# Kernel optimization log

Measured on AMD Instinct MI355X. Metric: run time of the kernel, lower is better.

The kernel has to match this reference:

```python
import jax, jax.numpy as jnp
import numpy as np

N_NODES = 100000
N_EDGES = 1600000
D = 128


def setup_inputs() -> dict:
    key = jax.random.key(0)
    ks = jax.random.split(key, 10)
    features = jax.random.normal(ks[0], (N_NODES, D), dtype=jnp.float32)
    edge_index = jax.random.randint(ks[1], (2, N_EDGES), 0, N_NODES, dtype=jnp.int64)
    edge_weight = jax.random.uniform(ks[2], (N_EDGES,), dtype=jnp.float32)
    scale = 1.0 / np.sqrt(D)
    W1 = jax.random.normal(ks[3], (D, D), dtype=jnp.float32) * scale
    b1 = jnp.zeros((D,), dtype=jnp.float32)
    a1 = jnp.full((D,), 0.25, dtype=jnp.float32)  # PReLU init
    W2 = jax.random.normal(ks[4], (D, D), dtype=jnp.float32) * scale
    b2 = jnp.zeros((D,), dtype=jnp.float32)
    a2 = jnp.full((D,), 0.25, dtype=jnp.float32)
    return {"features": features, "edge_index": edge_index, "edge_weight": edge_weight,
            "W1": W1, "b1": b1, "a1": a1, "W2": W2, "b2": b2, "a2": a2}


def _gcn_norm(edge_index, edge_weight, n_nodes):
    # PyG GCNConv default: add self-loops (weight 1), symmetric normalization.
    src, dst = edge_index[0], edge_index[1]
    loop = jnp.arange(n_nodes, dtype=src.dtype)
    src = jnp.concatenate([src, loop])
    dst = jnp.concatenate([dst, loop])
    w = jnp.concatenate([edge_weight, jnp.ones((n_nodes,), edge_weight.dtype)])
    deg = jax.ops.segment_sum(w, dst, num_segments=n_nodes)  # in-degree (target)
    dis = jnp.where(deg > 0, jax.lax.rsqrt(deg), 0.0)
    norm = dis[src] * w * dis[dst]  # [E + N]
    return src, dst, norm


def _gcn_layer(x, W, b, src, dst, norm, n_nodes):
    h = x @ W                                 # [N, D] dense GEMM first (PyG order)
    msg = h[src] * norm[:, None]              # gather + scale, [E+N, D]
    out = jax.ops.segment_sum(msg, dst, num_segments=n_nodes)
    return out + b


def _prelu(x, a):
    return jnp.where(x >= 0, x, a * x)


def reference(features, edge_index, edge_weight, W1, b1, a1, W2, b2, a2):
    n = features.shape[0]
    src, dst, norm = _gcn_norm(edge_index, edge_weight, n)
    # dropout is identity in eval mode
    x = _prelu(_gcn_layer(features, W1, b1, src, dst, norm, n), a1)
    x = _prelu(_gcn_layer(x, W2, b2, src, dst, norm, n), a2)
    return x
```

## Files before the change

kernel.cpp:

```cpp
#include <hip/hip_runtime.h>
#include <cstdint>

#define NN 100000
#define NE 1600000
#define DD 128
#define NB 250
#define BSZ 400

typedef unsigned int uint;
typedef unsigned short ushort;
typedef unsigned long long u64;

typedef __attribute__((ext_vector_type(8))) short short8;
typedef __attribute__((ext_vector_type(4))) float floatx4;

__device__ inline uint f2bf(float f) {
    uint u = __float_as_uint(f);
    return (u + 0x7fffu + ((u >> 16) & 1u)) >> 16;
}


__global__ __launch_bounds__(256) void zero_bc(uint* __restrict__ bc) {
    if (threadIdx.x < NB) bc[threadIdx.x] = 0u;
}

__global__ __launch_bounds__(256) void bucket_hist(const int* __restrict__ dst,
                                                   uint* __restrict__ bc) {
    __shared__ uint h[NB];
    int tid = threadIdx.x;
    if (tid < NB) h[tid] = 0u;
    __syncthreads();
    int e0 = blockIdx.x * 8192 + tid;
#pragma unroll
    for (int k = 0; k < 32; ++k) {
        int e = e0 + 256 * k;
        if (e < NE) atomicAdd(&h[(uint)dst[e] / BSZ], 1u);
    }
    __syncthreads();
    if (tid < NB && h[tid]) atomicAdd(&bc[tid], h[tid]);
}

__global__ __launch_bounds__(256) void bucket_prefix(const uint* __restrict__ bc,
                                                     uint* __restrict__ bbase,
                                                     uint* __restrict__ bcur) {
    int lane = threadIdx.x;
    if (lane < 64) {
        uint v[4], s = 0;
#pragma unroll
        for (int k = 0; k < 4; ++k) {
            int i = lane * 4 + k;
            v[k] = (i < NB) ? bc[i] : 0u;
            s += v[k];
        }
        uint inc = s;
#pragma unroll
        for (int d = 1; d < 64; d <<= 1) {
            uint t = __shfl_up(inc, (unsigned)d, 64);
            if (lane >= d) inc += t;
        }
        uint run = inc - s;
#pragma unroll
        for (int k = 0; k < 4; ++k) {
            int i = lane * 4 + k;
            if (i < NB) { bbase[i] = run; bcur[i] = run; run += v[k]; }
        }
        if (lane == 63) bbase[NB] = run;
    }
}

__global__ __launch_bounds__(256) void bucket_append(const int* __restrict__ src,
                                                     const int* __restrict__ dst,
                                                     const float* __restrict__ w,
                                                     uint* __restrict__ bcur,
                                                     int2* __restrict__ etmp) {
    __shared__ uint h[NB];
    __shared__ uint res[NB];
    int tid = threadIdx.x;
    if (tid < NB) h[tid] = 0u;
    __syncthreads();
    int e0 = blockIdx.x * 4096 + tid;
    uint rank[16], bkt[16];
#pragma unroll
    for (int k = 0; k < 16; ++k) {
        int e = e0 + 256 * k;
        if (e < NE) {
            uint b = (uint)dst[e] / BSZ;
            bkt[k] = b;
            rank[k] = atomicAdd(&h[b], 1u);
        } else bkt[k] = 0xffffffffu;
    }
    __syncthreads();
    if (tid < NB) res[tid] = h[tid] ? atomicAdd(&bcur[tid], h[tid]) : 0u;
    __syncthreads();
#pragma unroll
    for (int k = 0; k < 16; ++k) {
        if (bkt[k] != 0xffffffffu) {
            int e = e0 + 256 * k;
            uint dl = (uint)dst[e] - bkt[k] * BSZ;
            uint wq = (uint)(w[e] * 8388608.0f);
            if (wq > 8388607u) wq = 8388607u;
            etmp[res[bkt[k]] + rank[k]] = make_int2(src[e], (int)((dl << 23) | wq));
        }
    }
}

__global__ __launch_bounds__(256) void bucket_build(const int2* __restrict__ etmp,
                                                    const uint* __restrict__ bbase,
                                                    float* __restrict__ dis,
                                                    int* __restrict__ hist_g,
                                                    int* __restrict__ rowstart,
                                                    int2* __restrict__ edges) {
    __shared__ u64   wc[BSZ];
    __shared__ uint  cur[BSZ];
    __shared__ float disl[BSZ];
    int tid = threadIdx.x;
    int b = blockIdx.x;
    int n0 = b * BSZ;
    for (int i = tid; i < BSZ; i += 256) wc[i] = 0ull;
    __syncthreads();
    uint base = bbase[b], end = bbase[b + 1];
    for (uint i = base + tid; i < end; i += 256) {
        uint y = (uint)etmp[i].y;
        uint dl = y >> 23;
        atomicAdd(&wc[dl], ((u64)1 << 40) | (u64)(y & 0x7fffffu));
    }
    __syncthreads();
    if (tid < 64) {
        uint v[7], s = 0;
#pragma unroll
        for (int k = 0; k < 7; ++k) {
            int i = tid * 7 + k;
            v[k] = (i < BSZ) ? (uint)(wc[i] >> 40) : 0u;
            s += v[k];
        }
        uint inc = s;
#pragma unroll
        for (int d = 1; d < 64; d <<= 1) {
            uint t = __shfl_up(inc, (unsigned)d, 64);
            if (tid >= d) inc += t;
        }
        uint run = inc - s;
#pragma unroll
        for (int k = 0; k < 7; ++k) {
            int i = tid * 7 + k;
            if (i < BSZ) { cur[i] = run; run += v[k]; }
        }
    }
    __syncthreads();
    for (int i = tid; i < BSZ; i += 256) {
        u64 v = wc[i];
        float wsum = (float)(v & 0xffffffffffull) * (1.0f / 8388608.0f);
        float ds = rsqrtf(1.0f + wsum);
        disl[i] = ds;
        dis[n0 + i] = ds;
        hist_g[n0 + i] = (int)(v >> 40);
        rowstart[n0 + i] = (int)(base + cur[i]);
    }
    __syncthreads();
    for (uint i = base + tid; i < end; i += 256) {
        int2 e = etmp[i];
        uint y = (uint)e.y;
        uint dl = y >> 23;
        float wv = (float)(y & 0x7fffffu) * (1.0f / 8388608.0f);
        uint p = atomicAdd(&cur[dl], 1u);
        float nrm = wv * disl[dl];
        edges[base + p] = make_int2(e.x, __float_as_int(nrm));
    }
}

#define WTS 136
#define NTILES ((NN + 63) / 64)

template <bool AF32>
__global__ __launch_bounds__(256) void gemm_mfma(const void* __restrict__ Xv,
                                                 const float* __restrict__ W,
                                                 const float* __restrict__ dis,
                                                 ushort* __restrict__ HB) {
    __shared__ ushort Wt[DD * WTS];
    int tid = threadIdx.x;
#pragma unroll
    for (int it = 0; it < 16; ++it) {
        int flat = (tid + it * 256) * 4;
        int k = flat >> 7, n = flat & 127;
        float4 wv = *(const float4*)&W[flat];
        Wt[(n + 0) * WTS + k] = (ushort)f2bf(wv.x);
        Wt[(n + 1) * WTS + k] = (ushort)f2bf(wv.y);
        Wt[(n + 2) * WTS + k] = (ushort)f2bf(wv.z);
        Wt[(n + 3) * WTS + k] = (ushort)f2bf(wv.w);
    }
    __syncthreads();

    int wave = tid >> 6, lane = tid & 63;
    int q = lane >> 4, l16 = lane & 15;

    for (int tile = blockIdx.x; tile < NTILES; tile += gridDim.x) {
        int row0 = tile * 64 + wave * 16;

        int arow = row0 + l16;
        if (arow >= NN) arow = NN - 1;
        short8 afr[4];
        if (AF32) {
            const float* xr = (const float*)Xv + (size_t)arow * DD + q * 8;
#pragma unroll
            for (int ks = 0; ks < 4; ++ks) {
                float4 f0 = *(const float4*)(xr + ks * 32);
                float4 f1 = *(const float4*)(xr + ks * 32 + 4);
                uint4 u;
                u.x = f2bf(f0.x) | (f2bf(f0.y) << 16);
                u.y = f2bf(f0.z) | (f2bf(f0.w) << 16);
                u.z = f2bf(f1.x) | (f2bf(f1.y) << 16);
                u.w = f2bf(f1.z) | (f2bf(f1.w) << 16);
                afr[ks] = __builtin_bit_cast(short8, u);
            }
        } else {
            const ushort* xr = (const ushort*)Xv + (size_t)arow * DD + q * 8;
#pragma unroll
            for (int ks = 0; ks < 4; ++ks)
                afr[ks] = *(const short8*)(xr + ks * 32);
        }

        floatx4 acc[8];
#pragma unroll
        for (int ct = 0; ct < 8; ++ct) acc[ct] = (floatx4)(0.0f);

#pragma unroll
        for (int ct = 0; ct < 8; ++ct) {
            const ushort* wp = &Wt[(ct * 16 + l16) * WTS + q * 8];
#pragma unroll
            for (int ks = 0; ks < 4; ++ks) {
                short8 bfr = *(const short8*)(wp + ks * 32);
                acc[ct] = __builtin_amdgcn_mfma_f32_16x16x32_bf16(afr[ks], bfr, acc[ct], 0, 0, 0);
            }
        }

#pragma unroll
        for (int reg = 0; reg < 4; ++reg) {
            int r = row0 + q * 4 + reg;
            if (r < NN) {
                float ds = dis[r];
                ushort* orow = HB + (size_t)r * DD + l16;
#pragma unroll
                for (int ct = 0; ct < 8; ++ct)
                    orow[ct * 16] = (ushort)f2bf(acc[ct][reg] * ds);
            }
        }
    }
}

template <bool BF16OUT>
__global__ __launch_bounds__(256) void gather_finalize(const ushort* __restrict__ hb,
                                                       const int2* __restrict__ edges,
                                                       const int* __restrict__ rowstart,
                                                       const int* __restrict__ hist,
                                                       const float* __restrict__ dis,
                                                       const float* __restrict__ b,
                                                       const float* __restrict__ a,
                                                       void* __restrict__ xout) {
    int wid = __builtin_amdgcn_readfirstlane(threadIdx.x >> 6);
    int lane = threadIdx.x & 63;
    int node = blockIdx.x * 4 + wid;
    uint lane4 = (uint)lane * 4u;

    int rs  = rowstart[node];
    int cnt = hist[node];
    float ds = dis[node];
    const int2* ep = edges + rs;
    const char* hbase = (const char*)hb;

    uint su = *(const uint*)(hbase + ((uint)node << 8) + lane4);
    float2 acc0, acc1, acc2, acc3;
    acc0.x = __uint_as_float(su << 16) * ds;
    acc0.y = __uint_as_float(su & 0xffff0000u) * ds;
    acc1 = make_float2(0.f, 0.f);
    acc2 = make_float2(0.f, 0.f);
    acc3 = make_float2(0.f, 0.f);

    int full = cnt >> 4;
    int t = 0;
    for (; t < full; ++t) {
        int2 e[16];
#pragma unroll
        for (int k = 0; k < 16; ++k) e[k] = ep[t * 16 + k];
#pragma unroll
        for (int k = 0; k < 16; ++k) {
            uint voff = ((uint)e[k].x << 8) + lane4;
            uint g = *(const uint*)(hbase + voff);
            float nrm = __int_as_float(e[k].y);
            float2* ac = (k & 3) == 0 ? &acc0 : (k & 3) == 1 ? &acc1 : (k & 3) == 2 ? &acc2 : &acc3;
            ac->x += __uint_as_float(g << 16) * nrm;
            ac->y += __uint_as_float(g & 0xffff0000u) * nrm;
        }
    }
    int remn = cnt & 15;
    if (remn) {
        int2 e[16];
#pragma unroll
        for (int k = 0; k < 16; ++k) e[k] = ep[t * 16 + k];
#pragma unroll
        for (int k = 0; k < 16; ++k) {
            bool live = k < remn;
            uint sidx = live ? (uint)e[k].x : 0u;
            float nrm = live ? __int_as_float(e[k].y) : 0.0f;
            uint voff = (sidx << 8) + lane4;
            uint g = *(const uint*)(hbase + voff);
            float2* ac = (k & 3) == 0 ? &acc0 : (k & 3) == 1 ? &acc1 : (k & 3) == 2 ? &acc2 : &acc3;
            ac->x += __uint_as_float(g << 16) * nrm;
            ac->y += __uint_as_float(g & 0xffff0000u) * nrm;
        }
    }

    float2 bb = ((const float2*)b)[lane];
    float2 aa = ((const float2*)a)[lane];
    float r0 = acc0.x + acc1.x + acc2.x + acc3.x + bb.x;
    float r1 = acc0.y + acc1.y + acc2.y + acc3.y + bb.y;
    r0 = r0 >= 0.f ? r0 : aa.x * r0;
    r1 = r1 >= 0.f ? r1 : aa.y * r1;
    if (BF16OUT) {
        ((uint*)xout)[(size_t)node * 64 + lane] = f2bf(r0) | (f2bf(r1) << 16);
    } else {
        float2 o; o.x = r0; o.y = r1;
        ((float2*)xout)[(size_t)node * 64 + lane] = o;
    }
}

extern "C" void kernel_launch(void* const* d_in, const int* in_sizes, int n_in,
                              void* d_out, int out_size, void* d_ws, size_t ws_size,
                              hipStream_t stream) {
    const float* feat = (const float*)d_in[0];
    const int*   ei   = (const int*)d_in[1];
    const float* ew   = (const float*)d_in[2];
    const float* W1   = (const float*)d_in[3];
    const float* b1   = (const float*)d_in[4];
    const float* a1   = (const float*)d_in[5];
    const float* W2   = (const float*)d_in[6];
    const float* b2   = (const float*)d_in[7];
    const float* a2   = (const float*)d_in[8];
    float* out = (float*)d_out;

    const int* srcp = ei;
    const int* dstp = ei + NE;

    char* wsb = (char*)d_ws;
    size_t off = 0;
    uint* bc     = (uint*)(wsb + off); off += 4096;
    uint* bbase  = (uint*)(wsb + off); off += 4096;
    uint* bcur   = (uint*)(wsb + off); off += 4096;
    float* dis   = (float*)(wsb + off); off += 4ull * NN;
    int* hist    = (int*)(wsb + off); off += 4ull * NN;
    int* rowstart= (int*)(wsb + off); off += 4ull * NN;
    int2* etmp   = (int2*)(wsb + off); off += 8ull * NE;
    int2* edges  = (int2*)(wsb + off); off += 8ull * NE;
    ushort* hb   = (ushort*)(wsb + off); off += 2ull * NN * DD;
    ushort* x1b  = (ushort*)(wsb + off); off += 2ull * NN * DD;

    zero_bc<<<1, 256, 0, stream>>>(bc);
    bucket_hist<<<(NE + 8191) / 8192, 256, 0, stream>>>(dstp, bc);
    bucket_prefix<<<1, 256, 0, stream>>>(bc, bbase, bcur);
    bucket_append<<<(NE + 4095) / 4096, 256, 0, stream>>>(srcp, dstp, ew, bcur, etmp);
    bucket_build<<<NB, 256, 0, stream>>>(etmp, bbase, dis, hist, rowstart, edges);

    const int gemm_blocks = (NTILES + 1) / 2;
    const int gath_blocks = NN / 4;

    gemm_mfma<true><<<gemm_blocks, 256, 0, stream>>>(feat, W1, dis, hb);
    gather_finalize<true><<<gath_blocks, 256, 0, stream>>>(hb, edges, rowstart, hist, dis, b1, a1, x1b);
    gemm_mfma<false><<<gemm_blocks, 256, 0, stream>>>(x1b, W2, dis, hb);
    gather_finalize<false><<<gath_blocks, 256, 0, stream>>>(hb, edges, rowstart, hist, dis, b2, a2, out);
}
```

Before: 364.8 us.

## Process two nodes per wavefront in gather and drop global histogram atomics

The gather kernel now handles two destination nodes per wavefront, interleaving their edge loads and bf16 row gathers so more independent memory requests are in flight per wave, with all rows (including tails) handled through a single predicated loop. The bucket histogram writes per-block partial counts that the prefix kernel sums, which removes the zeroing kernel and the global atomics. The cost is more registers per wave, lower occupancy, and divergence-like waste when the two nodes have very different degrees.

```diff
diff --git a/kernel.cpp b/kernel.cpp
--- a/kernel.cpp
+++ b/kernel.cpp
@@ -6,6 +6,7 @@
 #define DD 128
 #define NB 250
 #define BSZ 400
+#define NHB ((NE + 8191) / 8192)
 
 typedef unsigned int uint;
 typedef unsigned short ushort;
@@ -20,12 +21,8 @@
 }
 
 
-__global__ __launch_bounds__(256) void zero_bc(uint* __restrict__ bc) {
-    if (threadIdx.x < NB) bc[threadIdx.x] = 0u;
-}
-
 __global__ __launch_bounds__(256) void bucket_hist(const int* __restrict__ dst,
-                                                   uint* __restrict__ bc) {
+                                                   uint* __restrict__ bcp) {
     __shared__ uint h[NB];
     int tid = threadIdx.x;
     if (tid < NB) h[tid] = 0u;
@@ -37,19 +34,27 @@
         if (e < NE) atomicAdd(&h[(uint)dst[e] / BSZ], 1u);
     }
     __syncthreads();
-    if (tid < NB && h[tid]) atomicAdd(&bc[tid], h[tid]);
-}
-
-__global__ __launch_bounds__(256) void bucket_prefix(const uint* __restrict__ bc,
+    if (tid < NB) bcp[blockIdx.x * 256 + tid] = h[tid];
+}
+
+__global__ __launch_bounds__(256) void bucket_prefix(const uint* __restrict__ bcp,
                                                      uint* __restrict__ bbase,
                                                      uint* __restrict__ bcur) {
-    int lane = threadIdx.x;
+    __shared__ uint cnt[NB];
+    int tid = threadIdx.x;
+    if (tid < NB) {
+        uint s = 0;
+        for (int j = 0; j < NHB; ++j) s += bcp[j * 256 + tid];
+        cnt[tid] = s;
+    }
+    __syncthreads();
+    int lane = tid;
     if (lane < 64) {
         uint v[4], s = 0;
 #pragma unroll
         for (int k = 0; k < 4; ++k) {
             int i = lane * 4 + k;
-            v[k] = (i < NB) ? bc[i] : 0u;
+            v[k] = (i < NB) ? cnt[i] : 0u;
             s += v[k];
         }
         uint inc = s;
@@ -258,68 +263,91 @@
                                                        void* __restrict__ xout) {
     int wid = __builtin_amdgcn_readfirstlane(threadIdx.x >> 6);
     int lane = threadIdx.x & 63;
-    int node = blockIdx.x * 4 + wid;
+    int nodeA = blockIdx.x * 8 + wid * 2;
+    int nodeB = nodeA + 1;
     uint lane4 = (uint)lane * 4u;
-
-    int rs  = rowstart[node];
-    int cnt = hist[node];
-    float ds = dis[node];
-    const int2* ep = edges + rs;
     const char* hbase = (const char*)hb;
 
-    uint su = *(const uint*)(hbase + ((uint)node << 8) + lane4);
-    float2 acc0, acc1, acc2, acc3;
-    acc0.x = __uint_as_float(su << 16) * ds;
-    acc0.y = __uint_as_float(su & 0xffff0000u) * ds;
-    acc1 = make_float2(0.f, 0.f);
-    acc2 = make_float2(0.f, 0.f);
-    acc3 = make_float2(0.f, 0.f);
-
-    int full = cnt >> 4;
-    int t = 0;
-    for (; t < full; ++t) {
-        int2 e[16];
-#pragma unroll
-        for (int k = 0; k < 16; ++k) e[k] = ep[t * 16 + k];
+    int rsA  = rowstart[nodeA];
+    int rsB  = rowstart[nodeB];
+    int cntA = hist[nodeA];
+    int cntB = hist[nodeB];
+    float dsA = dis[nodeA];
+    float dsB = dis[nodeB];
+    const int2* epA = edges + rsA;
+    const int2* epB = edges + rsB;
+
+    uint suA = *(const uint*)(hbase + ((size_t)(uint)nodeA << 8) + lane4);
+    uint suB = *(const uint*)(hbase + ((size_t)(uint)nodeB << 8) + lane4);
+    float2 a0, a1, a2, a3, b0, b1, b2, b3;
+    a0.x = __uint_as_float(suA << 16) * dsA;
+    a0.y = __uint_as_float(suA & 0xffff0000u) * dsA;
+    b0.x = __uint_as_float(suB << 16) * dsB;
+    b0.y = __uint_as_float(suB & 0xffff0000u) * dsB;
+    a1 = make_float2(0.f, 0.f); a2 = a1; a3 = a1;
+    b1 = a1; b2 = a1; b3 = a1;
+
+    int nbA = (cntA + 15) >> 4;
+    int nbB = (cntB + 15) >> 4;
+    int nb = nbA > nbB ? nbA : nbB;
+
+    for (int t = 0; t < nb; ++t) {
+        int remA = cntA - t * 16;
+        int remB = cntB - t * 16;
+        int2 eA[16], eB[16];
+#pragma unroll
+        for (int k = 0; k < 16; ++k) eA[k] = epA[t * 16 + k];
+#pragma unroll
+        for (int k = 0; k < 16; ++k) eB[k] = epB[t * 16 + k];
+
+        uint gA[16], gB[16];
+        float nA[16], nB[16];
 #pragma unroll
         for (int k = 0; k < 16; ++k) {
-            uint voff = ((uint)e[k].x << 8) + lane4;
-            uint g = *(const uint*)(hbase + voff);
-            float nrm = __int_as_float(e[k].y);
-            float2* ac = (k & 3) == 0 ? &acc0 : (k & 3) == 1 ? &acc1 : (k & 3) == 2 ? &acc2 : &acc3;
-            ac->x += __uint_as_float(g << 16) * nrm;
-            ac->y += __uint_as_float(g & 0xffff0000u) * nrm;
-        }
-    }
-    int remn = cnt & 15;
-    if (remn) {
-        int2 e[16];
-#pragma unroll
-        for (int k = 0; k < 16; ++k) e[k] = ep[t * 16 + k];
+            bool live = k < remA;
+            uint s = live ? (uint)eA[k].x : 0u;
+            nA[k] = live ? __int_as_float(eA[k].y) : 0.0f;
+            gA[k] = *(const uint*)(hbase + ((size_t)s << 8) + lane4);
+        }
 #pragma unroll
         for (int k = 0; k < 16; ++k) {
-            bool live = k < remn;
-            uint sidx = live ? (uint)e[k].x : 0u;
-            float nrm = live ? __int_as_float(e[k].y) : 0.0f;
-            uint voff = (sidx << 8) + lane4;
-            uint g = *(const uint*)(hbase + voff);
-            float2* ac = (k & 3) == 0 ? &acc0 : (k & 3) == 1 ? &acc1 : (k & 3) == 2 ? &acc2 : &acc3;
-            ac->x += __uint_as_float(g << 16) * nrm;
-            ac->y += __uint_as_float(g & 0xffff0000u) * nrm;
+            bool live = k < remB;
+            uint s = live ? (uint)eB[k].x : 0u;
+            nB[k] = live ? __int_as_float(eB[k].y) : 0.0f;
+            gB[k] = *(const uint*)(hbase + ((size_t)s << 8) + lane4);
+        }
+#pragma unroll
+        for (int k = 0; k < 16; ++k) {
+            float2* ac = (k & 3) == 0 ? &a0 : (k & 3) == 1 ? &a1 : (k & 3) == 2 ? &a2 : &a3;
+            ac->x += __uint_as_float(gA[k] << 16) * nA[k];
+            ac->y += __uint_as_float(gA[k] & 0xffff0000u) * nA[k];
+        }
+#pragma unroll
+        for (int k = 0; k < 16; ++k) {
+            float2* ac = (k & 3) == 0 ? &b0 : (k & 3) == 1 ? &b1 : (k & 3) == 2 ? &b2 : &b3;
+            ac->x += __uint_as_float(gB[k] << 16) * nB[k];
+            ac->y += __uint_as_float(gB[k] & 0xffff0000u) * nB[k];
         }
     }
 
     float2 bb = ((const float2*)b)[lane];
     float2 aa = ((const float2*)a)[lane];
-    float r0 = acc0.x + acc1.x + acc2.x + acc3.x + bb.x;
-    float r1 = acc0.y + acc1.y + acc2.y + acc3.y + bb.y;
-    r0 = r0 >= 0.f ? r0 : aa.x * r0;
-    r1 = r1 >= 0.f ? r1 : aa.y * r1;
+    float rA0 = a0.x + a1.x + a2.x + a3.x + bb.x;
+    float rA1 = a0.y + a1.y + a2.y + a3.y + bb.y;
+    float rB0 = b0.x + b1.x + b2.x + b3.x + bb.x;
+    float rB1 = b0.y + b1.y + b2.y + b3.y + bb.y;
+    rA0 = rA0 >= 0.f ? rA0 : aa.x * rA0;
+    rA1 = rA1 >= 0.f ? rA1 : aa.y * rA1;
+    rB0 = rB0 >= 0.f ? rB0 : aa.x * rB0;
+    rB1 = rB1 >= 0.f ? rB1 : aa.y * rB1;
     if (BF16OUT) {
-        ((uint*)xout)[(size_t)node * 64 + lane] = f2bf(r0) | (f2bf(r1) << 16);
+        ((uint*)xout)[(size_t)nodeA * 64 + lane] = f2bf(rA0) | (f2bf(rA1) << 16);
+        ((uint*)xout)[(size_t)nodeB * 64 + lane] = f2bf(rB0) | (f2bf(rB1) << 16);
     } else {
-        float2 o; o.x = r0; o.y = r1;
-        ((float2*)xout)[(size_t)node * 64 + lane] = o;
+        float2 oA; oA.x = rA0; oA.y = rA1;
+        float2 oB; oB.x = rB0; oB.y = rB1;
+        ((float2*)xout)[(size_t)nodeA * 64 + lane] = oA;
+        ((float2*)xout)[(size_t)nodeB * 64 + lane] = oB;
     }
 }
 
@@ -342,7 +370,7 @@
 
     char* wsb = (char*)d_ws;
     size_t off = 0;
-    uint* bc     = (uint*)(wsb + off); off += 4096;
+    uint* bcp    = (uint*)(wsb + off); off += 4ull * 256 * NHB;
     uint* bbase  = (uint*)(wsb + off); off += 4096;
     uint* bcur   = (uint*)(wsb + off); off += 4096;
     float* dis   = (float*)(wsb + off); off += 4ull * NN;
@@ -353,14 +381,13 @@
     ushort* hb   = (ushort*)(wsb + off); off += 2ull * NN * DD;
     ushort* x1b  = (ushort*)(wsb + off); off += 2ull * NN * DD;
 
-    zero_bc<<<1, 256, 0, stream>>>(bc);
-    bucket_hist<<<(NE + 8191) / 8192, 256, 0, stream>>>(dstp, bc);
-    bucket_prefix<<<1, 256, 0, stream>>>(bc, bbase, bcur);
+    bucket_hist<<<NHB, 256, 0, stream>>>(dstp, bcp);
+    bucket_prefix<<<1, 256, 0, stream>>>(bcp, bbase, bcur);
     bucket_append<<<(NE + 4095) / 4096, 256, 0, stream>>>(srcp, dstp, ew, bcur, etmp);
     bucket_build<<<NB, 256, 0, stream>>>(etmp, bbase, dis, hist, rowstart, edges);
 
     const int gemm_blocks = (NTILES + 1) / 2;
-    const int gath_blocks = NN / 4;
+    const int gath_blocks = NN / 8;
 
     gemm_mfma<true><<<gemm_blocks, 256, 0, stream>>>(feat, W1, dis, hb);
     gather_finalize<true><<<gath_blocks, 256, 0, stream>>>(hb, edges, rowstart, hist, dis, b1, a1, x1b);
```

Result: no change. 368.9 us (+1.1%).
